# Optimization experiments

Measured on AMD Instinct MI355X. Metric: run time of the kernel, lower is better.

The kernel has to match this reference:

```python
import jax, jax.numpy as jnp
import numpy as np

N, ND, NPAIR, KS = 131072, 32, 6, 3  # batch, dijetFeatures, 6 dijets, kernel=stride=3

def setup_inputs() -> dict:
    key = jax.random.key(0)
    k1, k2, k3, k4 = jax.random.split(key, 4)
    x = jax.random.normal(k1, (N, ND, 2 * NPAIR), dtype=jnp.float32)
    d = jax.random.normal(k2, (N, ND, NPAIR), dtype=jnp.float32)
    # Conv1d(nd, nd, 3, stride=3) params, torch layout [out_ch, in_ch, k]
    fan_in = ND * KS
    W = jax.random.normal(k3, (ND, ND, KS), dtype=jnp.float32) / np.float32(np.sqrt(fan_in))
    b = jax.random.normal(k4, (ND,), dtype=jnp.float32) * 0.01
    return {"x": x, "d": d, "W": W, "b": b}

def reference(x, d, W, b):
    n = x.shape[0]
    # reinforce interleave: (j0 j1 d0 | j2 j3 d1 | ...) -> [n, nd, 6, 3]
    # x[:, :, 2s:2s+2] followed by d[:, :, s] for each of the 6 slots.
    din = jnp.concatenate([x.reshape(n, ND, NPAIR, 2), d[..., None]], axis=3)
    # Conv1d kernel=stride=3 over the length-18 interleaved seq == per-slot contraction
    out = jnp.einsum('ncsk,ock->nos', din, W) + b[None, :, None]
    return out  # [n, nd, 6]
```

## Files before the change

### kernel.cpp

```cpp
#include <hip/hip_runtime.h>


#define ND 32
#define NPAIR 6
#define SPB 32
#define BT 192
#define OSTR 200

typedef __attribute__((ext_vector_type(8))) short bf16x8;
typedef __attribute__((ext_vector_type(4))) float f32x4;

union BU { unsigned u[4]; bf16x8 v; };

__device__ __forceinline__ unsigned pack2(float lo, float hi) {
    return __builtin_amdgcn_perm(__float_as_uint(hi), __float_as_uint(lo), 0x07060302u);
}

__global__ __launch_bounds__(BT) void dijet_mfma(
    const float* __restrict__ x,
    const float* __restrict__ d,
    const float* __restrict__ W,
    const float* __restrict__ bias,
    float* __restrict__ out,
    int N)
{
    __shared__ __align__(16) float obuf[SPB * OSTR];

    const int t    = threadIdx.x;
    const int n0   = blockIdx.x * SPB;
    const bool full = (n0 + SPB <= N);

    const int w     = t >> 6;
    const int l     = t & 63;
    const int row16 = l & 15;
    const int quad  = l >> 4;
    const int ct0   = w * 4;

    bf16x8 Af[2][3];
#pragma unroll
    for (int ot = 0; ot < 2; ++ot) {
        const float* wb = W + (ot * 16 + row16) * 96;
        const float* wq = wb + quad * 12;
#pragma unroll
        for (int ks = 0; ks < 2; ++ks) {
            BU b;
#pragma unroll
            for (int cc = 0; cc < 4; ++cc) {
                const float* p = wq + (16 * ks + cc) * 3;
                b.u[cc] = pack2(p[0], p[1]);
            }
            Af[ot][ks] = b.v;
        }
        const float* wq2 = wb + quad * 24 + 2;
        BU b2;
#pragma unroll
        for (int m = 0; m < 4; ++m)
            b2.u[m] = pack2(wq2[(2 * m) * 3], wq2[(2 * m + 1) * 3]);
        Af[ot][2] = b2.v;
    }

    float4 bv0 = *(const float4*)(bias + quad * 4);
    float4 bv1 = *(const float4*)(bias + 16 + quad * 4);
    f32x4 acc[4][2];
#pragma unroll
    for (int ct = 0; ct < 4; ++ct) {
        acc[ct][0] = (f32x4){bv0.x, bv0.y, bv0.z, bv0.w};
        acc[ct][1] = (f32x4){bv1.x, bv1.y, bv1.z, bv1.w};
    }

#pragma unroll
    for (int ct = 0; ct < 4; ++ct) {
        const int col = (ct0 + ct) * 16 + row16;
        const int ls  = col / 6;
        const int s   = col - ls * 6;
        const bool ok = full || (n0 + ls < N);

        const float* xp = x + (size_t)(n0 + ls) * 384 + quad * 48 + 2 * s;
        const float* dp = d + (size_t)(n0 + ls) * 192 + quad * 48 + s;

        float2 v0[4], v1[4];
        float  vd[8];
#pragma unroll
        for (int cc = 0; cc < 4; ++cc) {
            v0[cc] = ok ? *(const float2*)(xp + cc * 12)       : make_float2(0.f, 0.f);
            v1[cc] = ok ? *(const float2*)(xp + 192 + cc * 12) : make_float2(0.f, 0.f);
        }
#pragma unroll
        for (int j = 0; j < 8; ++j)
            vd[j] = ok ? dp[j * 6] : 0.f;

        BU b0, b1, b2;
#pragma unroll
        for (int cc = 0; cc < 4; ++cc) {
            b0.u[cc] = pack2(v0[cc].x, v0[cc].y);
            b1.u[cc] = pack2(v1[cc].x, v1[cc].y);
        }
#pragma unroll
        for (int m = 0; m < 4; ++m)
            b2.u[m] = pack2(vd[2 * m], vd[2 * m + 1]);

        acc[ct][0] = __builtin_amdgcn_mfma_f32_16x16x32_bf16(Af[0][0], b0.v, acc[ct][0], 0, 0, 0);
        acc[ct][0] = __builtin_amdgcn_mfma_f32_16x16x32_bf16(Af[0][1], b1.v, acc[ct][0], 0, 0, 0);
        acc[ct][0] = __builtin_amdgcn_mfma_f32_16x16x32_bf16(Af[0][2], b2.v, acc[ct][0], 0, 0, 0);
        acc[ct][1] = __builtin_amdgcn_mfma_f32_16x16x32_bf16(Af[1][0], b0.v, acc[ct][1], 0, 0, 0);
        acc[ct][1] = __builtin_amdgcn_mfma_f32_16x16x32_bf16(Af[1][1], b1.v, acc[ct][1], 0, 0, 0);
        acc[ct][1] = __builtin_amdgcn_mfma_f32_16x16x32_bf16(Af[1][2], b2.v, acc[ct][1], 0, 0, 0);
    }

#pragma unroll
    for (int ct = 0; ct < 4; ++ct) {
        const int col = (ct0 + ct) * 16 + row16;
        const int ls  = col / 6;
        const int s   = col - ls * 6;
        float* ob = obuf + ls * OSTR + s;
#pragma unroll
        for (int ot = 0; ot < 2; ++ot) {
            const int o0 = ot * 16 + quad * 4;
            ob[(o0 + 0) * NPAIR] = acc[ct][ot].x;
            ob[(o0 + 1) * NPAIR] = acc[ct][ot].y;
            ob[(o0 + 2) * NPAIR] = acc[ct][ot].z;
            ob[(o0 + 3) * NPAIR] = acc[ct][ot].w;
        }
    }

    __syncthreads();

    float* og = out + (size_t)n0 * (ND * NPAIR);
#pragma unroll
    for (int k = 0; k < 8; ++k) {
        const int F  = 4 * (t + k * BT);
        const int ns = F / 192;
        const int wi = F % 192;
        if (full || n0 + ns < N) {
            float4 v = *(const float4*)(obuf + ns * OSTR + wi);
            *(float4*)(og + ns * 192 + wi) = v;
        }
    }
}

extern "C" void kernel_launch(void* const* d_in, const int* in_sizes, int n_in,
                              void* d_out, int out_size, void* d_ws, size_t ws_size,
                              hipStream_t stream) {
    const float* x = (const float*)d_in[0];
    const float* d = (const float*)d_in[1];
    const float* W = (const float*)d_in[2];
    const float* b = (const float*)d_in[3];
    float* out = (float*)d_out;

    int N = in_sizes[0] / (ND * 2 * NPAIR);
    int blocks = (N + SPB - 1) / SPB;

    dijet_mfma<<<blocks, BT, 0, stream>>>(x, d, W, b, out, N);
}
```

Measured before the change: 391.9 us.

## Stage x/d tiles into LDS via direct global-to-LDS loads and prepack weights

Measured after the change: 362.4 us. 1.08x faster.

```diff
diff --git a/kernel.cpp b/kernel.cpp
--- a/kernel.cpp
+++ b/kernel.cpp
@@ -6,58 +6,102 @@
 #define SPB 32
 #define BT 192
 #define OSTR 200
+#define XBYTES (SPB * 1536)
+#define DBYTES (SPB * 768)
 
 typedef __attribute__((ext_vector_type(8))) short bf16x8;
 typedef __attribute__((ext_vector_type(4))) float f32x4;
+typedef unsigned int u32;
 
 union BU { unsigned u[4]; bf16x8 v; };
 
 __device__ __forceinline__ unsigned pack2(float lo, float hi) {
     return __builtin_amdgcn_perm(__float_as_uint(hi), __float_as_uint(lo), 0x07060302u);
+}
+__device__ __forceinline__ unsigned short bf16t(float v) {
+    return (unsigned short)(__float_as_uint(v) >> 16);
+}
+
+__device__ __forceinline__ void load_lds16(const void* g, void* l) {
+    __builtin_amdgcn_global_load_lds(
+        (const __attribute__((address_space(1))) u32*)g,
+        (__attribute__((address_space(3))) u32*)l, 16, 0, 0);
+}
+
+__global__ void dijet_prep(const float* __restrict__ W, uint4* __restrict__ ws) {
+    const int i = threadIdx.x;
+    const int f = i >> 6;
+    const int l = i & 63;
+    const int row16 = l & 15;
+    const int quad  = l >> 4;
+    const int ot = f / 3, ks = f % 3;
+    const float* wb = W + (ot * 16 + row16) * 96;
+    BU b;
+    if (ks < 2) {
+        const float* wq = wb + quad * 12;
+#pragma unroll
+        for (int cc = 0; cc < 4; ++cc) {
+            const float* p = wq + (16 * ks + cc) * 3;
+            b.u[cc] = pack2(p[0], p[1]);
+        }
+    } else {
+        const float* wq2 = wb + quad * 24 + 2;
+#pragma unroll
+        for (int m = 0; m < 4; ++m)
+            b.u[m] = pack2(wq2[(2 * m) * 3], wq2[(2 * m + 1) * 3]);
+    }
+    ws[f * 64 + l] = *(const uint4*)&b;
 }
 
 __global__ __launch_bounds__(BT) void dijet_mfma(
     const float* __restrict__ x,
     const float* __restrict__ d,
-    const float* __restrict__ W,
+    const uint4* __restrict__ ws,
     const float* __restrict__ bias,
     float* __restrict__ out,
     int N)
 {
-    __shared__ __align__(16) float obuf[SPB * OSTR];
+    __shared__ __align__(16) unsigned char smem[XBYTES + DBYTES];
 
     const int t    = threadIdx.x;
     const int n0   = blockIdx.x * SPB;
     const bool full = (n0 + SPB <= N);
 
-    const int w     = t >> 6;
+    const int wv    = t >> 6;
     const int l     = t & 63;
     const int row16 = l & 15;
     const int quad  = l >> 4;
-    const int ct0   = w * 4;
+    const int ct0   = wv * 4;
+
+    {
+        const size_t xmax = (size_t)N * 1536 - 1024;
+#pragma unroll
+        for (int i = 0; i < 16; ++i) {
+            const int ci = i * 3 + wv;
+            size_t goff = (size_t)n0 * 1536 + (size_t)ci * 1024;
+            if (!full && goff > xmax) goff = xmax;
+            load_lds16((const char*)x + goff + l * 16, smem + ci * 1024);
+        }
+    }
+    {
+        const size_t dmax = (size_t)N * 768 - 1024;
+#pragma unroll
+        for (int i = 0; i < 8; ++i) {
+            const int ci = i * 3 + wv;
+            size_t goff = (size_t)n0 * 768 + (size_t)ci * 1024;
+            if (!full && goff > dmax) goff = dmax;
+            load_lds16((const char*)d + goff + l * 16, smem + XBYTES + ci * 1024);
+        }
+    }
 
     bf16x8 Af[2][3];
 #pragma unroll
-    for (int ot = 0; ot < 2; ++ot) {
-        const float* wb = W + (ot * 16 + row16) * 96;
-        const float* wq = wb + quad * 12;
-#pragma unroll
-        for (int ks = 0; ks < 2; ++ks) {
-            BU b;
-#pragma unroll
-            for (int cc = 0; cc < 4; ++cc) {
-                const float* p = wq + (16 * ks + cc) * 3;
-                b.u[cc] = pack2(p[0], p[1]);
-            }
-            Af[ot][ks] = b.v;
-        }
-        const float* wq2 = wb + quad * 24 + 2;
-        BU b2;
-#pragma unroll
-        for (int m = 0; m < 4; ++m)
-            b2.u[m] = pack2(wq2[(2 * m) * 3], wq2[(2 * m + 1) * 3]);
-        Af[ot][2] = b2.v;
-    }
+    for (int ot = 0; ot < 2; ++ot)
+#pragma unroll
+        for (int ks = 0; ks < 3; ++ks) {
+            uint4 r = ws[(ot * 3 + ks) * 64 + l];
+            Af[ot][ks] = *(const bf16x8*)&r;
+        }
 
     float4 bv0 = *(const float4*)(bias + quad * 4);
     float4 bv1 = *(const float4*)(bias + 16 + quad * 4);
@@ -68,26 +112,28 @@
         acc[ct][1] = (f32x4){bv1.x, bv1.y, bv1.z, bv1.w};
     }
 
+    __syncthreads();
+
+    const float* xls = (const float*)smem;
+    const float* dls = (const float*)(smem + XBYTES);
 #pragma unroll
     for (int ct = 0; ct < 4; ++ct) {
         const int col = (ct0 + ct) * 16 + row16;
         const int ls  = col / 6;
         const int s   = col - ls * 6;
-        const bool ok = full || (n0 + ls < N);
-
-        const float* xp = x + (size_t)(n0 + ls) * 384 + quad * 48 + 2 * s;
-        const float* dp = d + (size_t)(n0 + ls) * 192 + quad * 48 + s;
+        const float* xp = xls + ls * 384 + quad * 48 + 2 * s;
+        const float* dp = dls + ls * 192 + quad * 48 + s;
 
         float2 v0[4], v1[4];
         float  vd[8];
 #pragma unroll
         for (int cc = 0; cc < 4; ++cc) {
-            v0[cc] = ok ? *(const float2*)(xp + cc * 12)       : make_float2(0.f, 0.f);
-            v1[cc] = ok ? *(const float2*)(xp + 192 + cc * 12) : make_float2(0.f, 0.f);
+            v0[cc] = *(const float2*)(xp + cc * 12);
+            v1[cc] = *(const float2*)(xp + 192 + cc * 12);
         }
 #pragma unroll
         for (int j = 0; j < 8; ++j)
-            vd[j] = ok ? dp[j * 6] : 0.f;
+            vd[j] = dp[j * 6];
 
         BU b0, b1, b2;
 #pragma unroll
@@ -107,6 +153,9 @@
         acc[ct][1] = __builtin_amdgcn_mfma_f32_16x16x32_bf16(Af[1][2], b2.v, acc[ct][1], 0, 0, 0);
     }
 
+    __syncthreads();
+
+    float* obuf = (float*)smem;
 #pragma unroll
     for (int ct = 0; ct < 4; ++ct) {
         const int col = (ct0 + ct) * 16 + row16;
@@ -150,5 +199,6 @@
     int N = in_sizes[0] / (ND * 2 * NPAIR);
     int blocks = (N + SPB - 1) / SPB;
 
-    dijet_mfma<<<blocks, BT, 0, stream>>>(x, d, W, b, out, N);
-}
+    dijet_prep<<<1, 384, 0, stream>>>(W, (uint4*)d_ws);
+    dijet_mfma<<<blocks, BT, 0, stream>>>(x, d, (const uint4*)d_ws, b, out, N);
+}
```
